# Optimization experiments

Hardware: AMD Instinct MI355X
Metric: run time of the kernel (lower is better)

## Reference

```python
import jax, jax.numpy as jnp
import numpy as np

NEG_SLOPE = 0.2  # PyG GATConv default leaky_relu slope
EPS = 1e-16


def setup_inputs() -> dict:
    key = jax.random.key(0)
    ks = jax.random.split(key, 8)
    N, E, F = 50000, 1600000, 128
    L, H, C = 3, 4, 32  # layers, heads, per-head channels; H*C == F
    Dh = 32             # MLP hidden (== hidden_channels)
    x = jax.random.normal(ks[0], (N, F), jnp.float32)
    edge_index = jax.random.randint(ks[1], (2, E), 0, N, jnp.int32)
    W = jax.random.normal(ks[2], (L, F, H * C), jnp.float32) * 0.1
    att_src = jax.random.normal(ks[3], (L, H, C), jnp.float32) * 0.1
    att_dst = jax.random.normal(ks[4], (L, H, C), jnp.float32) * 0.1
    b_conv = jnp.zeros((L, H * C), jnp.float32)
    W1 = jax.random.normal(ks[5], (F + H * C, Dh), jnp.float32) * 0.1
    b1 = jnp.zeros((Dh,), jnp.float32)
    W2 = jax.random.normal(ks[6], (Dh, 1), jnp.float32) * 0.1
    b2 = jnp.zeros((1,), jnp.float32)
    return {"x": x, "edge_index": edge_index, "W": W, "att_src": att_src,
            "att_dst": att_dst, "b_conv": b_conv, "W1": W1, "b1": b1,
            "W2": W2, "b2": b2}


def _gat_layer(x, src, dst, W, a_s, a_d, b, N):
    H, C = a_s.shape
    h = (x @ W).reshape(N, H, C)                      # [N,H,C]
    alpha_s = jnp.sum(h * a_s, axis=-1)               # [N,H]
    alpha_d = jnp.sum(h * a_d, axis=-1)               # [N,H]
    e = jax.nn.leaky_relu(alpha_s[src] + alpha_d[dst], NEG_SLOPE)  # [E,H]
    # segment softmax over incoming edges of each dst node
    m = jax.ops.segment_max(e, dst, num_segments=N)
    ex = jnp.exp(e - m[dst])
    s = jax.ops.segment_sum(ex, dst, num_segments=N)
    a = ex / (s[dst] + EPS)                           # [E,H]
    out = jax.ops.segment_sum(h[src] * a[:, :, None], dst, num_segments=N)
    return out.reshape(N, H * C) + b


def reference(x, edge_index, W, att_src, att_dst, b_conv, W1, b1, W2, b2):
    N = x.shape[0]
    loops = jnp.arange(N, dtype=edge_index.dtype)
    src = jnp.concatenate([edge_index[0], loops])  # PyG GATConv adds self loops
    dst = jnp.concatenate([edge_index[1], loops])
    x0 = x
    for l in range(W.shape[0]):
        x = _gat_layer(x, src, dst, W[l], att_src[l], att_dst[l], b_conv[l], N)
    h = jnp.concatenate([x, x0], axis=-1)
    h = jax.nn.relu(h @ W1 + b1)
    return jax.nn.sigmoid(h @ W2 + b2)
```

## Files before the change

### kernel.cpp

```cpp
#include <hip/hip_runtime.h>

#define NEG_SLOPE 0.2f
#define EPSF 1e-16f
#define SEG_SHIFT 13

typedef unsigned int uint;
typedef unsigned short ushort;
typedef __attribute__((ext_vector_type(8))) short short8;
typedef __attribute__((ext_vector_type(4))) float floatx4;
typedef __attribute__((ext_vector_type(4))) uint uintx4;

static __device__ __forceinline__ ushort f2bf(float f) {
    uint u = __float_as_uint(f);
    return (ushort)((u + 0x7FFFu + ((u >> 16) & 1u)) >> 16);
}
static __device__ __forceinline__ uint pack2(float a, float b) {
    return (uint)f2bf(a) | ((uint)f2bf(b) << 16);
}
static __device__ __forceinline__ float bf_lo(uint p) { return __uint_as_float(p << 16); }
static __device__ __forceinline__ float bf_hi(uint p) { return __uint_as_float(p & 0xFFFF0000u); }
static __device__ __forceinline__ short8 u2s8(uint4 v) {
    union { uint4 u; short8 s; } c; c.u = v; return c.s;
}
static __device__ __forceinline__ void load_lds16(const void* g, void* l) {
    __builtin_amdgcn_global_load_lds(
        (const __attribute__((address_space(1))) void*)g,
        (__attribute__((address_space(3))) void*)l, 16, 0, 0);
}

__global__ __launch_bounds__(256) void prep_count_kernel(
    const float* __restrict__ W, const float* __restrict__ W1,
    const float* __restrict__ x, uint4* __restrict__ Wp,
    uint4* __restrict__ W1p, uint4* __restrict__ xb,
    const int* __restrict__ ei, int E, int NB,
    int* __restrict__ bucket_count, int L, int N, int nbPrep)
{
    __shared__ int cnt[256];
    if ((int)blockIdx.x >= nbPrep) {
        cnt[threadIdx.x] = 0;
        __syncthreads();
        const int base = (blockIdx.x - nbPrep) * 2048 + threadIdx.x;
#pragma unroll
        for (int j = 0; j < 8; ++j) {
            int idx = base + j * 256;
            if (idx < E) atomicAdd(&cnt[ei[E + idx] >> 8], 1);
        }
        __syncthreads();
        int c = cnt[threadIdx.x];
        if ((int)threadIdx.x < NB && c) atomicAdd(&bucket_count[threadIdx.x], c);
        return;
    }
    int id = blockIdx.x * 256 + threadIdx.x;
    const int nW = L * 2048;
    const int nX = N * 16;
    if (id < nW) {
        int l = id >> 11, s = id & 2047;
        int chunk = s >> 7, col = s & 127;
        const float* wp = W + (size_t)l * 16384 + (chunk * 8) * 128 + col;
        uint4 pk;
        pk.x = pack2(wp[0],   wp[128]);
        pk.y = pack2(wp[256], wp[384]);
        pk.z = pack2(wp[512], wp[640]);
        pk.w = pack2(wp[768], wp[896]);
        Wp[id] = pk;
    } else if (id < nW + 1024) {
        int s = id - nW;
        int chunk = s >> 5, col = s & 31;
        const float* wp = W1 + (chunk * 8) * 32 + col;
        uint4 pk;
        pk.x = pack2(wp[0],   wp[32]);
        pk.y = pack2(wp[64],  wp[96]);
        pk.z = pack2(wp[128], wp[160]);
        pk.w = pack2(wp[192], wp[224]);
        W1p[s] = pk;
    } else if (id < nW + 1024 + nX) {
        int xid = id - nW - 1024;
        int row = xid >> 4, c8 = xid & 15;
        const float4* xp = (const float4*)(x + (size_t)row * 128 + c8 * 8);
        float4 v0 = xp[0], v1 = xp[1];
        uint4 pk;
        pk.x = pack2(v0.x, v0.y); pk.y = pack2(v0.z, v0.w);
        pk.z = pack2(v1.x, v1.y); pk.w = pack2(v1.z, v1.w);
        xb[xid] = pk;
    }
}

#define GA_LDS_BYTES ((2048 + 1040) * 16)
__global__ __launch_bounds__(256) void gemm_alpha_kernel(
    const uint4* __restrict__ xb, const uint4* __restrict__ Wp,
    const float* __restrict__ att_s, const float* __restrict__ att_d,
    uint* __restrict__ h2, float* __restrict__ alpha_s,
    float* __restrict__ alpha_d, int N)
{
    __shared__ __align__(16) char smraw[GA_LDS_BYTES];
    uint4* sW = (uint4*)smraw;
    uint4* sX = sW + 2048;
    float* sD = (float*)smraw;

    const int t = threadIdx.x;
    const int wb = t & ~63;
    const int rowBase = blockIdx.x * 64;

#pragma unroll
    for (int i = 0; i < 8; ++i)
        load_lds16(Wp + i * 256 + t, sW + i * 256 + wb);

#pragma unroll
    for (int i = 0; i < 4; ++i) {
        int f = t + i * 256;
        int row = f >> 4, c8 = f & 15;
        uint4 v = make_uint4(0u, 0u, 0u, 0u);
        if (rowBase + row < N) v = xb[(size_t)(rowBase + row) * 16 + c8];
        sX[c8 * 65 + row] = v;
    }
    __syncthreads();

    const int w = t >> 6, lane = t & 63, q = lane >> 4, l15 = lane & 15;
    short8 a[4];
#pragma unroll
    for (int s = 0; s < 4; ++s)
        a[s] = u2s8(sX[(4 * s + q) * 65 + 16 * w + l15]);

    floatx4 acc[8];
#pragma unroll
    for (int ct = 0; ct < 8; ++ct) acc[ct] = (floatx4){0.f, 0.f, 0.f, 0.f};
#pragma unroll
    for (int ct = 0; ct < 8; ++ct) {
#pragma unroll
        for (int s = 0; s < 4; ++s) {
            short8 b = u2s8(sW[(4 * s + q) * 128 + 16 * ct + l15]);
            acc[ct] = __builtin_amdgcn_mfma_f32_16x16x32_bf16(a[s], b, acc[ct], 0, 0, 0);
        }
    }
    __syncthreads();

#pragma unroll
    for (int ct = 0; ct < 8; ++ct) {
#pragma unroll
        for (int r = 0; r < 4; ++r)
            sD[(16 * w + 4 * q + r) * 129 + 16 * ct + l15] = acc[ct][r];
    }
    __syncthreads();

#pragma unroll
    for (int i = 0; i < 4; ++i) {
        int slot = t + i * 256;
        int row = slot >> 4, c8 = slot & 15;
        if (rowBase + row < N) {
            const float* dp = &sD[row * 129 + c8 * 8];
            uint4 o;
            o.x = pack2(dp[0], dp[1]); o.y = pack2(dp[2], dp[3]);
            o.z = pack2(dp[4], dp[5]); o.w = pack2(dp[6], dp[7]);
            ((uint4*)h2)[(size_t)(rowBase + row) * 16 + c8] = o;
        }
    }
    {
        int row = t & 63, head = t >> 6;
        if (rowBase + row < N) {
            const float* dp = &sD[row * 129 + head * 32];
            const float* asp = att_s + head * 32;
            const float* adp = att_d + head * 32;
            float ps = 0.f, pd = 0.f;
#pragma unroll
            for (int c = 0; c < 32; ++c) { float v = dp[c]; ps += v * asp[c]; pd += v * adp[c]; }
            alpha_s[(size_t)(rowBase + row) * 4 + head] = ps;
            alpha_d[(size_t)(rowBase + row) * 4 + head] = pd;
        }
    }
}

__global__ __launch_bounds__(256) void bucket_scan_kernel(
    const int* __restrict__ bucket_count, int NB,
    int* __restrict__ bucket_base, int* __restrict__ bucket_cursor,
    int* __restrict__ row_start, int N)
{
    __shared__ int s[256];
    const int t = threadIdx.x;
    int v = (t < NB) ? bucket_count[t] : 0;
    s[t] = v;
    __syncthreads();
    for (int off = 1; off < 256; off <<= 1) {
        int x = s[t];
        int a = (t >= off) ? s[t - off] : 0;
        __syncthreads();
        s[t] = x + a;
        __syncthreads();
    }
    int ex = s[t] - v;
    if (t < NB) { bucket_base[t] = ex; bucket_cursor[t] = ex; }
    if (t == 255) { bucket_base[NB] = s[255]; row_start[N] = s[255]; }
}

__global__ __launch_bounds__(256) void distribute_kernel(
    const int* __restrict__ ei, int E, int NB,
    int* __restrict__ bucket_cursor, uint* __restrict__ bdata)
{
    __shared__ int cnt[256];
    __shared__ int bbase[256];
    cnt[threadIdx.x] = 0;
    __syncthreads();
    const int base = blockIdx.x * 2048 + threadIdx.x;
    int srcs[8], dsts[8], rank[8];
#pragma unroll
    for (int j = 0; j < 8; ++j) {
        int idx = base + j * 256;
        if (idx < E) {
            srcs[j] = ei[idx];
            dsts[j] = ei[E + idx];
            rank[j] = atomicAdd(&cnt[dsts[j] >> 8], 1);
        } else dsts[j] = -1;
    }
    __syncthreads();
    {
        int c = cnt[threadIdx.x];
        bbase[threadIdx.x] = ((int)threadIdx.x < NB && c) ? atomicAdd(&bucket_cursor[threadIdx.x], c) : 0;
    }
    __syncthreads();
#pragma unroll
    for (int j = 0; j < 8; ++j) {
        if (dsts[j] >= 0) {
            int b = dsts[j] >> 8;
            bdata[bbase[b] + rank[j]] = (uint)srcs[j] | ((uint)(dsts[j] & 255) << 16);
        }
    }
}

#define BCAP 12800
__global__ __launch_bounds__(256) void bucket_csr_kernel(
    const uint* __restrict__ bdata, const int* __restrict__ bucket_base,
    int* __restrict__ row_start, ushort* __restrict__ csr_src, int N)
{
    __shared__ int hist[2048];
    __shared__ int cur[2048];
    __shared__ int scn[256];
    __shared__ ushort buf[BCAP];
    const int b = blockIdx.x;
    const int t = threadIdx.x;
    const int beg = bucket_base[b];
    const int sz = bucket_base[b + 1] - beg;
#pragma unroll
    for (int j = 0; j < 8; ++j) hist[t * 8 + j] = 0;
    __syncthreads();
    for (int i = t; i < sz; i += 256) {
        uint d = bdata[beg + i];
        int key = (int)((d >> 16) << 3) | (int)((d & 0xFFFFu) >> SEG_SHIFT);
        atomicAdd(&hist[key], 1);
    }
    __syncthreads();
    int local[8]; int s = 0;
#pragma unroll
    for (int j = 0; j < 8; ++j) { local[j] = hist[t * 8 + j]; s += local[j]; }
    scn[t] = s;
    __syncthreads();
    for (int off = 1; off < 256; off <<= 1) {
        int x = scn[t];
        int a = (t >= off) ? scn[t - off] : 0;
        __syncthreads();
        scn[t] = x + a;
        __syncthreads();
    }
    int run = scn[t] - s;
#pragma unroll
    for (int j = 0; j < 8; ++j) { cur[t * 8 + j] = run; run += local[j]; }
    __syncthreads();
    int node = b * 256 + t;
    if (node < N) row_start[node] = beg + cur[t << 3];
    __syncthreads();
    if (sz <= BCAP) {
        for (int i = t; i < sz; i += 256) {
            uint d = bdata[beg + i];
            int key = (int)((d >> 16) << 3) | (int)((d & 0xFFFFu) >> SEG_SHIFT);
            int pos = atomicAdd(&cur[key], 1);
            buf[pos] = (ushort)(d & 0xFFFFu);
        }
        __syncthreads();
        for (int i = t; i < sz; i += 256) csr_src[beg + i] = buf[i];
    } else {
        for (int i = t; i < sz; i += 256) {
            uint d = bdata[beg + i];
            int key = (int)((d >> 16) << 3) | (int)((d & 0xFFFFu) >> SEG_SHIFT);
            int pos = atomicAdd(&cur[key], 1);
            csr_src[beg + pos] = (ushort)(d & 0xFFFFu);
        }
    }
}

__global__ __launch_bounds__(256) void agg_csr_kernel(
    const ushort* __restrict__ csr_src, const int* __restrict__ row_start,
    const float* __restrict__ alpha_s, const float* __restrict__ alpha_d,
    const uint* __restrict__ h2, const float* __restrict__ b,
    uint* __restrict__ outb, int N)
{
    const int g = (blockIdx.x * 256 + threadIdx.x) >> 4;
    const int l = threadIdx.x & 15;
    if (g >= N) return;
    const int head = l >> 2;
    const uint4* h4 = (const uint4*)h2;

    const float ad = alpha_d[g * 4 + head];

    float e = alpha_s[g * 4 + head] + ad;
    e = e > 0.f ? e : NEG_SLOPE * e;
    float ex = __expf(e);
    uint4 q = h4[(size_t)g * 16 + l];
    float a0 = ex * bf_lo(q.x), a1 = ex * bf_hi(q.x);
    float a2 = ex * bf_lo(q.y), a3 = ex * bf_hi(q.y);
    float a4 = ex * bf_lo(q.z), a5 = ex * bf_hi(q.z);
    float a6 = ex * bf_lo(q.w), a7 = ex * bf_hi(q.w);
    float sx = ex;

    const int beg = row_start[g];
    const int end = row_start[g + 1];
    int k = beg;
    for (; k + 4 <= end; k += 4) {
        int s0 = csr_src[k], s1 = csr_src[k + 1];
        int s2 = csr_src[k + 2], s3 = csr_src[k + 3];
        uint4 q0 = h4[(size_t)s0 * 16 + l];
        uint4 q1 = h4[(size_t)s1 * 16 + l];
        uint4 q2 = h4[(size_t)s2 * 16 + l];
        uint4 q3 = h4[(size_t)s3 * 16 + l];
        float e0 = alpha_s[s0 * 4 + head] + ad;
        float e1 = alpha_s[s1 * 4 + head] + ad;
        float e2 = alpha_s[s2 * 4 + head] + ad;
        float e3 = alpha_s[s3 * 4 + head] + ad;
        e0 = e0 > 0.f ? e0 : NEG_SLOPE * e0;
        e1 = e1 > 0.f ? e1 : NEG_SLOPE * e1;
        e2 = e2 > 0.f ? e2 : NEG_SLOPE * e2;
        e3 = e3 > 0.f ? e3 : NEG_SLOPE * e3;
        float x0 = __expf(e0), x1 = __expf(e1);
        float x2 = __expf(e2), x3 = __expf(e3);
        a0 += x0 * bf_lo(q0.x) + x1 * bf_lo(q1.x) + x2 * bf_lo(q2.x) + x3 * bf_lo(q3.x);
        a1 += x0 * bf_hi(q0.x) + x1 * bf_hi(q1.x) + x2 * bf_hi(q2.x) + x3 * bf_hi(q3.x);
        a2 += x0 * bf_lo(q0.y) + x1 * bf_lo(q1.y) + x2 * bf_lo(q2.y) + x3 * bf_lo(q3.y);
        a3 += x0 * bf_hi(q0.y) + x1 * bf_hi(q1.y) + x2 * bf_hi(q2.y) + x3 * bf_hi(q3.y);
        a4 += x0 * bf_lo(q0.z) + x1 * bf_lo(q1.z) + x2 * bf_lo(q2.z) + x3 * bf_lo(q3.z);
        a5 += x0 * bf_hi(q0.z) + x1 * bf_hi(q1.z) + x2 * bf_hi(q2.z) + x3 * bf_hi(q3.z);
        a6 += x0 * bf_lo(q0.w) + x1 * bf_lo(q1.w) + x2 * bf_lo(q2.w) + x3 * bf_lo(q3.w);
        a7 += x0 * bf_hi(q0.w) + x1 * bf_hi(q1.w) + x2 * bf_hi(q2.w) + x3 * bf_hi(q3.w);
        sx += x0 + x1 + x2 + x3;
    }
    for (; k < end; ++k) {
        int s0 = csr_src[k];
        float e0 = alpha_s[s0 * 4 + head] + ad;
        uint4 q0 = h4[(size_t)s0 * 16 + l];
        e0 = e0 > 0.f ? e0 : NEG_SLOPE * e0;
        float x0 = __expf(e0);
        a0 += x0 * bf_lo(q0.x); a1 += x0 * bf_hi(q0.x);
        a2 += x0 * bf_lo(q0.y); a3 += x0 * bf_hi(q0.y);
        a4 += x0 * bf_lo(q0.z); a5 += x0 * bf_hi(q0.z);
        a6 += x0 * bf_lo(q0.w); a7 += x0 * bf_hi(q0.w);
        sx += x0;
    }
    const float inv = 1.f / (sx + EPSF);
    const float4 b0 = ((const float4*)b)[l * 2];
    const float4 b1 = ((const float4*)b)[l * 2 + 1];
    uintx4 o;
    o.x = pack2(b0.x + a0 * inv, b0.y + a1 * inv);
    o.y = pack2(b0.z + a2 * inv, b0.w + a3 * inv);
    o.z = pack2(b1.x + a4 * inv, b1.y + a5 * inv);
    o.w = pack2(b1.z + a6 * inv, b1.w + a7 * inv);
    __builtin_nontemporal_store(o, (uintx4*)(outb + (size_t)g * 64 + l * 4));
}

__global__ __launch_bounds__(256) void mlp_kernel(
    const uint4* __restrict__ xb3, const uint4* __restrict__ xb0,
    const uint4* __restrict__ W1p, const float* __restrict__ b1,
    const float* __restrict__ W2, const float* __restrict__ b2,
    float* __restrict__ out, int N)
{
    __shared__ __align__(16) uint4 sA[32 * 65];
    __shared__ __align__(16) uint4 sB[32 * 32];
    const int t = threadIdx.x;
    const int wb = t & ~63;
    const int rowBase = blockIdx.x * 64;

#pragma unroll
    for (int i = 0; i < 4; ++i)
        load_lds16(W1p + i * 256 + t, sB + i * 256 + wb);
#pragma unroll
    for (int i = 0; i < 8; ++i) {
        int f = t + i * 256;
        int c = f & 31, row = f >> 5;
        uint4 v = make_uint4(0u, 0u, 0u, 0u);
        int grow = rowBase + row;
        if (grow < N)
            v = (c < 16) ? xb3[(size_t)grow * 16 + c]
                         : xb0[(size_t)grow * 16 + (c - 16)];
        sA[c * 65 + row] = v;
    }
    __syncthreads();

    const int w = t >> 6, lane = t & 63, q = lane >> 4, l15 = lane & 15;
    floatx4 acc0 = (floatx4){0.f, 0.f, 0.f, 0.f};
    floatx4 acc1 = (floatx4){0.f, 0.f, 0.f, 0.f};
#pragma unroll
    for (int s = 0; s < 8; ++s) {
        short8 a = u2s8(sA[(4 * s + q) * 65 + 16 * w + l15]);
        acc0 = __builtin_amdgcn_mfma_f32_16x16x32_bf16(a, u2s8(sB[(4 * s + q) * 32 + l15]), acc0, 0, 0, 0);
        acc1 = __builtin_amdgcn_mfma_f32_16x16x32_bf16(a, u2s8(sB[(4 * s + q) * 32 + 16 + l15]), acc1, 0, 0, 0);
    }
    const float b1a = b1[l15], b1b = b1[16 + l15];
    const float w2a = W2[l15], w2b = W2[16 + l15];
    const float b2v = b2[0];
#pragma unroll
    for (int r = 0; r < 4; ++r) {
        int row = rowBase + 16 * w + 4 * q + r;
        float v0 = acc0[r] + b1a; v0 = v0 > 0.f ? v0 : 0.f;
        float v1 = acc1[r] + b1b; v1 = v1 > 0.f ? v1 : 0.f;
        float p = v0 * w2a + v1 * w2b;
        p += __shfl_xor(p, 1);
        p += __shfl_xor(p, 2);
        p += __shfl_xor(p, 4);
        p += __shfl_xor(p, 8);
        if (l15 == 0 && row < N)
            out[row] = 1.f / (1.f + __expf(-(p + b2v)));
    }
}

extern "C" void kernel_launch(void* const* d_in, const int* in_sizes, int n_in,
                              void* d_out, int out_size, void* d_ws, size_t ws_size,
                              hipStream_t stream)
{
    const float* x       = (const float*)d_in[0];
    const int*   ei      = (const int*)d_in[1];
    const float* W       = (const float*)d_in[2];
    const float* att_src = (const float*)d_in[3];
    const float* att_dst = (const float*)d_in[4];
    const float* b_conv  = (const float*)d_in[5];
    const float* W1      = (const float*)d_in[6];
    const float* b1      = (const float*)d_in[7];
    const float* W2      = (const float*)d_in[8];
    const float* b2      = (const float*)d_in[9];
    float* outp = (float*)d_out;

    const int N = in_sizes[0] / 128;
    const int E = in_sizes[1] / 2;
    const int L = in_sizes[2] / (128 * 128);
    const int NB = (N + 255) >> 8;

    char* ws = (char*)d_ws;
    uint*  h2      = (uint*)ws;
    uint4* xb0     = (uint4*)(h2 + (size_t)N * 64);
    uint4* xb      = xb0 + (size_t)N * 16;
    float* alpha_s = (float*)(xb + (size_t)N * 16);
    float* alpha_d = alpha_s + (size_t)N * 4;
    uint4* Wp      = (uint4*)(alpha_d + (size_t)N * 4);
    uint4* W1p     = Wp + (size_t)L * 2048;
    int* bucket_count  = (int*)(W1p + 1024);
    int* bucket_base   = bucket_count + 256;
    int* bucket_cursor = bucket_base + 260;
    int* row_start     = bucket_cursor + 256;
    uint* bdata        = (uint*)(row_start + N + 1);
    ushort* csr_src    = (ushort*)(bdata + E);

    const int nbE = (E + 2047) / 2048;
    const int prepItems = L * 2048 + 1024 + N * 16;
    const int nbPrep = (prepItems + 255) / 256;

    (void)hipMemsetAsync(bucket_count, 0, 256 * sizeof(int), stream);

    prep_count_kernel<<<nbPrep + nbE, 256, 0, stream>>>(
        W, W1, x, Wp, W1p, xb0, ei, E, NB, bucket_count, L, N, nbPrep);

    bucket_scan_kernel<<<1, 256, 0, stream>>>(bucket_count, NB, bucket_base,
                                              bucket_cursor, row_start, N);
    distribute_kernel<<<nbE, 256, 0, stream>>>(ei, E, NB, bucket_cursor, bdata);
    bucket_csr_kernel<<<NB, 256, 0, stream>>>(bdata, bucket_base, row_start,
                                              csr_src, N);

    for (int l = 0; l < L; ++l) {
        const uint4* xin = (l == 0) ? xb0 : xb;
        const uint4* Wl  = Wp + (size_t)l * 2048;
        const float* asl = att_src + (size_t)l * 128;
        const float* adl = att_dst + (size_t)l * 128;
        const float* bl  = b_conv + (size_t)l * 128;

        gemm_alpha_kernel<<<(N + 63) / 64, 256, 0, stream>>>(
            xin, Wl, asl, adl, h2, alpha_s, alpha_d, N);

        agg_csr_kernel<<<(N * 16 + 255) / 256, 256, 0, stream>>>(
            csr_src, row_start, alpha_s, alpha_d, h2, bl, (uint*)xb, N);
    }

    mlp_kernel<<<(N + 63) / 64, 256, 0, stream>>>(
        xb, xb0, W1p, b1, W2, b2, outp, N);
}
```

Before: 359.8 us.

## Epilogue from MFMA registers, finer CSR source sort, larger distribute tiles

The GEMM epilogue now swaps the MFMA operands so each lane holds one node's features. It packs and stores h directly from registers and computes the attention logits with cross-lane shuffles, which removes the LDS staging buffer and two barriers. The CSR build sorts each destination's sources into 16 sub-segments instead of 8, aiming for better gather locality in aggregation. The distribute kernel processes 4096 edges per block, and the aggregation kernel uses 32-bit byte-offset addressing. Costs include more LDS for the histogram, more registers in distribute, and strided 8-byte stores of h.

```diff
diff --git a/kernel.cpp b/kernel.cpp
--- a/kernel.cpp
+++ b/kernel.cpp
@@ -2,7 +2,7 @@
 
 #define NEG_SLOPE 0.2f
 #define EPSF 1e-16f
-#define SEG_SHIFT 13
+#define SEG_SHIFT 12
 
 typedef unsigned int uint;
 typedef unsigned short ushort;
@@ -85,17 +85,14 @@
     }
 }
 
-#define GA_LDS_BYTES ((2048 + 1040) * 16)
 __global__ __launch_bounds__(256) void gemm_alpha_kernel(
     const uint4* __restrict__ xb, const uint4* __restrict__ Wp,
     const float* __restrict__ att_s, const float* __restrict__ att_d,
     uint* __restrict__ h2, float* __restrict__ alpha_s,
     float* __restrict__ alpha_d, int N)
 {
-    __shared__ __align__(16) char smraw[GA_LDS_BYTES];
-    uint4* sW = (uint4*)smraw;
-    uint4* sX = sW + 2048;
-    float* sD = (float*)smraw;
+    __shared__ __align__(16) uint4 sW[2048];
+    __shared__ __align__(16) uint4 sX[16 * 65];
 
     const int t = threadIdx.x;
     const int wb = t & ~63;
@@ -116,10 +113,10 @@
     __syncthreads();
 
     const int w = t >> 6, lane = t & 63, q = lane >> 4, l15 = lane & 15;
-    short8 a[4];
+    short8 xf[4];
 #pragma unroll
     for (int s = 0; s < 4; ++s)
-        a[s] = u2s8(sX[(4 * s + q) * 65 + 16 * w + l15]);
+        xf[s] = u2s8(sX[(4 * s + q) * 65 + 16 * w + l15]);
 
     floatx4 acc[8];
 #pragma unroll
@@ -128,44 +125,45 @@
     for (int ct = 0; ct < 8; ++ct) {
 #pragma unroll
         for (int s = 0; s < 4; ++s) {
-            short8 b = u2s8(sW[(4 * s + q) * 128 + 16 * ct + l15]);
-            acc[ct] = __builtin_amdgcn_mfma_f32_16x16x32_bf16(a[s], b, acc[ct], 0, 0, 0);
-        }
-    }
-    __syncthreads();
-
-#pragma unroll
-    for (int ct = 0; ct < 8; ++ct) {
-#pragma unroll
-        for (int r = 0; r < 4; ++r)
-            sD[(16 * w + 4 * q + r) * 129 + 16 * ct + l15] = acc[ct][r];
-    }
-    __syncthreads();
-
-#pragma unroll
-    for (int i = 0; i < 4; ++i) {
-        int slot = t + i * 256;
-        int row = slot >> 4, c8 = slot & 15;
-        if (rowBase + row < N) {
-            const float* dp = &sD[row * 129 + c8 * 8];
-            uint4 o;
-            o.x = pack2(dp[0], dp[1]); o.y = pack2(dp[2], dp[3]);
-            o.z = pack2(dp[4], dp[5]); o.w = pack2(dp[6], dp[7]);
-            ((uint4*)h2)[(size_t)(rowBase + row) * 16 + c8] = o;
-        }
-    }
-    {
-        int row = t & 63, head = t >> 6;
-        if (rowBase + row < N) {
-            const float* dp = &sD[row * 129 + head * 32];
-            const float* asp = att_s + head * 32;
-            const float* adp = att_d + head * 32;
-            float ps = 0.f, pd = 0.f;
-#pragma unroll
-            for (int c = 0; c < 32; ++c) { float v = dp[c]; ps += v * asp[c]; pd += v * adp[c]; }
-            alpha_s[(size_t)(rowBase + row) * 4 + head] = ps;
-            alpha_d[(size_t)(rowBase + row) * 4 + head] = pd;
-        }
+            short8 wf = u2s8(sW[(4 * s + q) * 128 + 16 * ct + l15]);
+            acc[ct] = __builtin_amdgcn_mfma_f32_16x16x32_bf16(wf, xf[s], acc[ct], 0, 0, 0);
+        }
+    }
+
+    const int node = rowBase + 16 * w + l15;
+    if (node < N) {
+        uint2* hp = (uint2*)(h2 + (size_t)node * 64);
+#pragma unroll
+        for (int ct = 0; ct < 8; ++ct) {
+            uint2 o;
+            o.x = pack2(acc[ct][0], acc[ct][1]);
+            o.y = pack2(acc[ct][2], acc[ct][3]);
+            hp[(8 * ct + 2 * q) >> 1] = o;
+        }
+    }
+    float ps[4], pd[4];
+#pragma unroll
+    for (int hd = 0; hd < 4; ++hd) {
+        const float4 as0 = *(const float4*)(att_s + 32 * hd + 4 * q);
+        const float4 as1 = *(const float4*)(att_s + 32 * hd + 16 + 4 * q);
+        const float4 ad0 = *(const float4*)(att_d + 32 * hd + 4 * q);
+        const float4 ad1 = *(const float4*)(att_d + 32 * hd + 16 + 4 * q);
+        floatx4 c0 = acc[2 * hd], c1 = acc[2 * hd + 1];
+        ps[hd] = c0[0] * as0.x + c0[1] * as0.y + c0[2] * as0.z + c0[3] * as0.w
+               + c1[0] * as1.x + c1[1] * as1.y + c1[2] * as1.z + c1[3] * as1.w;
+        pd[hd] = c0[0] * ad0.x + c0[1] * ad0.y + c0[2] * ad0.z + c0[3] * ad0.w
+               + c1[0] * ad1.x + c1[1] * ad1.y + c1[2] * ad1.z + c1[3] * ad1.w;
+    }
+#pragma unroll
+    for (int hd = 0; hd < 4; ++hd) {
+        ps[hd] += __shfl_xor(ps[hd], 16);
+        ps[hd] += __shfl_xor(ps[hd], 32);
+        pd[hd] += __shfl_xor(pd[hd], 16);
+        pd[hd] += __shfl_xor(pd[hd], 32);
+    }
+    if (node < N) {
+        alpha_s[(size_t)node * 4 + q] = ps[q];
+        alpha_d[(size_t)node * 4 + q] = pd[q];
     }
 }
 
@@ -199,10 +197,10 @@
     __shared__ int bbase[256];
     cnt[threadIdx.x] = 0;
     __syncthreads();
-    const int base = blockIdx.x * 2048 + threadIdx.x;
-    int srcs[8], dsts[8], rank[8];
-#pragma unroll
-    for (int j = 0; j < 8; ++j) {
+    const int base = blockIdx.x * 4096 + threadIdx.x;
+    int srcs[16], dsts[16], rank[16];
+#pragma unroll
+    for (int j = 0; j < 16; ++j) {
         int idx = base + j * 256;
         if (idx < E) {
             srcs[j] = ei[idx];
@@ -217,7 +215,7 @@
     }
     __syncthreads();
 #pragma unroll
-    for (int j = 0; j < 8; ++j) {
+    for (int j = 0; j < 16; ++j) {
         if (dsts[j] >= 0) {
             int b = dsts[j] >> 8;
             bdata[bbase[b] + rank[j]] = (uint)srcs[j] | ((uint)(dsts[j] & 255) << 16);
@@ -230,8 +228,8 @@
     const uint* __restrict__ bdata, const int* __restrict__ bucket_base,
     int* __restrict__ row_start, ushort* __restrict__ csr_src, int N)
 {
-    __shared__ int hist[2048];
-    __shared__ int cur[2048];
+    __shared__ int hist[4096];
+    __shared__ int cur[4096];
     __shared__ int scn[256];
     __shared__ ushort buf[BCAP];
     const int b = blockIdx.x;
@@ -239,17 +237,17 @@
     const int beg = bucket_base[b];
     const int sz = bucket_base[b + 1] - beg;
 #pragma unroll
-    for (int j = 0; j < 8; ++j) hist[t * 8 + j] = 0;
+    for (int j = 0; j < 16; ++j) hist[t * 16 + j] = 0;
     __syncthreads();
     for (int i = t; i < sz; i += 256) {
         uint d = bdata[beg + i];
-        int key = (int)((d >> 16) << 3) | (int)((d & 0xFFFFu) >> SEG_SHIFT);
+        int key = (int)((d >> 16) << 4) | (int)((d & 0xFFFFu) >> SEG_SHIFT);
         atomicAdd(&hist[key], 1);
     }
     __syncthreads();
-    int local[8]; int s = 0;
-#pragma unroll
-    for (int j = 0; j < 8; ++j) { local[j] = hist[t * 8 + j]; s += local[j]; }
+    int local[16]; int s = 0;
+#pragma unroll
+    for (int j = 0; j < 16; ++j) { local[j] = hist[t * 16 + j]; s += local[j]; }
     scn[t] = s;
     __syncthreads();
     for (int off = 1; off < 256; off <<= 1) {
@@ -261,15 +259,15 @@
     }
     int run = scn[t] - s;
 #pragma unroll
-    for (int j = 0; j < 8; ++j) { cur[t * 8 + j] = run; run += local[j]; }
+    for (int j = 0; j < 16; ++j) { cur[t * 16 + j] = run; run += local[j]; }
     __syncthreads();
     int node = b * 256 + t;
-    if (node < N) row_start[node] = beg + cur[t << 3];
+    if (node < N) row_start[node] = beg + cur[t << 4];
     __syncthreads();
     if (sz <= BCAP) {
         for (int i = t; i < sz; i += 256) {
             uint d = bdata[beg + i];
-            int key = (int)((d >> 16) << 3) | (int)((d & 0xFFFFu) >> SEG_SHIFT);
+            int key = (int)((d >> 16) << 4) | (int)((d & 0xFFFFu) >> SEG_SHIFT);
             int pos = atomicAdd(&cur[key], 1);
             buf[pos] = (ushort)(d & 0xFFFFu);
         }
@@ -278,7 +276,7 @@
     } else {
         for (int i = t; i < sz; i += 256) {
             uint d = bdata[beg + i];
-            int key = (int)((d >> 16) << 3) | (int)((d & 0xFFFFu) >> SEG_SHIFT);
+            int key = (int)((d >> 16) << 4) | (int)((d & 0xFFFFu) >> SEG_SHIFT);
             int pos = atomicAdd(&cur[key], 1);
             csr_src[beg + pos] = (ushort)(d & 0xFFFFu);
         }
@@ -295,14 +293,14 @@
     const int l = threadIdx.x & 15;
     if (g >= N) return;
     const int head = l >> 2;
-    const uint4* h4 = (const uint4*)h2;
+    const char* hbase = (const char*)h2 + (size_t)l * 16;
 
     const float ad = alpha_d[g * 4 + head];
 
     float e = alpha_s[g * 4 + head] + ad;
     e = e > 0.f ? e : NEG_SLOPE * e;
     float ex = __expf(e);
-    uint4 q = h4[(size_t)g * 16 + l];
+    uint4 q = *(const uint4*)(hbase + (uint)g * 256u);
     float a0 = ex * bf_lo(q.x), a1 = ex * bf_hi(q.x);
     float a2 = ex * bf_lo(q.y), a3 = ex * bf_hi(q.y);
     float a4 = ex * bf_lo(q.z), a5 = ex * bf_hi(q.z);
@@ -313,12 +311,12 @@
     const int end = row_start[g + 1];
     int k = beg;
     for (; k + 4 <= end; k += 4) {
-        int s0 = csr_src[k], s1 = csr_src[k + 1];
-        int s2 = csr_src[k + 2], s3 = csr_src[k + 3];
-        uint4 q0 = h4[(size_t)s0 * 16 + l];
-        uint4 q1 = h4[(size_t)s1 * 16 + l];
-        uint4 q2 = h4[(size_t)s2 * 16 + l];
-        uint4 q3 = h4[(size_t)s3 * 16 + l];
+        uint s0 = csr_src[k], s1 = csr_src[k + 1];
+        uint s2 = csr_src[k + 2], s3 = csr_src[k + 3];
+        uint4 q0 = *(const uint4*)(hbase + s0 * 256u);
+        uint4 q1 = *(const uint4*)(hbase + s1 * 256u);
+        uint4 q2 = *(const uint4*)(hbase + s2 * 256u);
+        uint4 q3 = *(const uint4*)(hbase + s3 * 256u);
         float e0 = alpha_s[s0 * 4 + head] + ad;
         float e1 = alpha_s[s1 * 4 + head] + ad;
         float e2 = alpha_s[s2 * 4 + head] + ad;
@@ -340,9 +338,9 @@
         sx += x0 + x1 + x2 + x3;
     }
     for (; k < end; ++k) {
-        int s0 = csr_src[k];
+        uint s0 = csr_src[k];
         float e0 = alpha_s[s0 * 4 + head] + ad;
-        uint4 q0 = h4[(size_t)s0 * 16 + l];
+        uint4 q0 = *(const uint4*)(hbase + s0 * 256u);
         e0 = e0 > 0.f ? e0 : NEG_SLOPE * e0;
         float x0 = __expf(e0);
         a0 += x0 * bf_lo(q0.x); a1 += x0 * bf_hi(q0.x);
@@ -453,18 +451,19 @@
     uint* bdata        = (uint*)(row_start + N + 1);
     ushort* csr_src    = (ushort*)(bdata + E);
 
-    const int nbE = (E + 2047) / 2048;
+    const int nbEc = (E + 2047) / 2048;
+    const int nbEd = (E + 4095) / 4096;
     const int prepItems = L * 2048 + 1024 + N * 16;
     const int nbPrep = (prepItems + 255) / 256;
 
     (void)hipMemsetAsync(bucket_count, 0, 256 * sizeof(int), stream);
 
-    prep_count_kernel<<<nbPrep + nbE, 256, 0, stream>>>(
+    prep_count_kernel<<<nbPrep + nbEc, 256, 0, stream>>>(
         W, W1, x, Wp, W1p, xb0, ei, E, NB, bucket_count, L, N, nbPrep);
 
     bucket_scan_kernel<<<1, 256, 0, stream>>>(bucket_count, NB, bucket_base,
                                               bucket_cursor, row_start, N);
-    distribute_kernel<<<nbE, 256, 0, stream>>>(ei, E, NB, bucket_cursor, bdata);
+    distribute_kernel<<<nbEd, 256, 0, stream>>>(ei, E, NB, bucket_cursor, bdata);
     bucket_csr_kernel<<<NB, 256, 0, stream>>>(bdata, bucket_base, row_start,
                                               csr_src, N);
 
```

Measured after the change: 368.9 us. 1.03x slower.
